# Optimization experiments

Measured on AMD Instinct MI355X. Metric: run time of the kernel, lower is better.

## Reference

```python
import jax, jax.numpy as jnp
import numpy as np

# Dims: B latent vectors processed through T sequential LALR-state calls.
B, T = 4096, 128      # batch of latent vecs, timesteps
NL = 256              # n_latent (scaled up from default 100)
NS = 64               # number of LALR states with learned layers
NO = 32               # output tokens per state (Linear(n_latent, n_out))
V = 64                # len(terminals): size of scattered output vector


def setup_inputs() -> dict:
    key = jax.random.key(0)
    ks = jax.random.split(key, 7)
    return {
        "latent0": jax.random.normal(ks[0], (B, NL), jnp.float32),
        "W1": jax.random.normal(ks[1], (NS, NL, NL), jnp.float32) / np.sqrt(NL).astype(np.float32),
        "b1": jax.random.normal(ks[2], (NS, NL), jnp.float32) * 0.01,
        "W2": jax.random.normal(ks[3], (NS, NO, NL), jnp.float32) / np.sqrt(NL).astype(np.float32),
        "b2": jax.random.normal(ks[4], (NS, NO), jnp.float32) * 0.01,
        "state_seq": jax.random.randint(ks[5], (T,), 0, NS, jnp.int32),
        "out_idx": jax.random.randint(ks[6], (NS, NO), 0, V, jnp.int32),
    }


def reference(latent0, W1, b1, W2, b2, state_seq, out_idx):
    """Per-timestep LALR state call:
       newlatent = tanh(Linear(x));
       probs     = softmax(Linear(newlatent));
       output    = IndicesExpansion: scatter probs into zeros(V) at out_idx[state].
    State weights are gathered by state id; batch is processed jointly."""
    def step(x, s):
        w1, bb1 = W1[s], b1[s]            # [NL,NL], [NL]
        w2, bb2 = W2[s], b2[s]            # [NO,NL], [NO]
        idx = out_idx[s]                  # [NO]
        x_new = jnp.tanh(x @ w1.T + bb1)                       # [B, NL]
        probs = jax.nn.softmax(x_new @ w2.T + bb2, axis=-1)    # [B, NO]
        # IndicesExpansionLayer: zero vector of size V, set vals at indices
        y = jnp.zeros((x.shape[0], V), x.dtype).at[:, idx].set(probs)
        return x_new, y

    final_latent, ys = jax.lax.scan(step, latent0, state_seq)  # ys: [T, B, V]
    return jnp.transpose(ys, (1, 0, 2))  # [B, T, V]
```

## Files before the change

kernel.cpp:

```cpp
#include <hip/hip_runtime.h>

#define B_  4096
#define T_  128
#define NL  256
#define NS  64
#define NO  32
#define V_  64
#define RB  16
#define NBLK (B_ / RB)

typedef __bf16 bf16;
typedef bf16  bf16x8 __attribute__((ext_vector_type(8)));
typedef bf16  bf16x4 __attribute__((ext_vector_type(4)));
typedef float f32x4  __attribute__((ext_vector_type(4)));

#define MF(a, b, c) __builtin_amdgcn_mfma_f32_16x16x32_bf16(a, b, c, 0, 0, 0)

#define LGKM_BARRIER() asm volatile("s_waitcnt lgkmcnt(0)\n\ts_barrier" ::: "memory")

#define GLOAD(dst, ptr, off) \
    asm volatile("global_load_dwordx4 %0, %1, off offset:" #off \
                 : "=v"(dst) : "v"(ptr))

template <int TSHIFT>
__global__ void split_w_frag(const float* __restrict__ src,
                             bf16* __restrict__ hi, bf16* __restrict__ lo,
                             int total4) {
    int t4 = blockIdx.x * blockDim.x + threadIdx.x;
    if (t4 >= total4) return;
    const int jb   = (t4 & 1) * 4;
    const int L    = (t4 >> 1) & 63;
    const int ks   = (t4 >> 7) & 7;
    const int rest = t4 >> 10;
    const int t    = rest & ((1 << TSHIFT) - 1);
    const int s    = rest >> TSHIFT;
    const int row  = ((s << TSHIFT) + t) * 16 + (L & 15);
    const int k    = ks * 32 + (L >> 4) * 8 + jb;
    const float4 v = *(const float4*)(src + (size_t)row * NL + k);
    float vv[4] = {v.x, v.y, v.z, v.w};
    bf16x4 h, l;
#pragma unroll
    for (int e = 0; e < 4; e++) {
        bf16 hh = (bf16)vv[e];
        h[e] = hh;
        l[e] = (bf16)(vv[e] - (float)hh);
    }
    *(bf16x4*)(hi + (size_t)t4 * 4) = h;
    *(bf16x4*)(lo + (size_t)t4 * 4) = l;
}

__global__ void inv_kernel(const int* __restrict__ out_idx, int* __restrict__ inv) {
    int t = blockIdx.x * blockDim.x + threadIdx.x;
    if (t >= NS * V_) return;
    int s = t >> 6, v = t & 63;
    int jf = -1;
#pragma unroll
    for (int j = 0; j < NO; j++)
        if (out_idx[(s << 5) | j] == v) jf = j;
    inv[t] = jf;
}

__device__ __forceinline__ float fast_tanh(float z) {
    float e = __expf(2.0f * z);
    return 1.0f - 2.0f / (e + 1.0f);
}

__device__ __forceinline__ int xaddr(int t, int q, int n) {
    return ((t >> 1) * 512) + (((t & 1) * 2 + (q >> 1)) * 128) + n * 8 + (q & 1) * 4;
}

__launch_bounds__(1024, 4)
__global__ void lalr_main(const float* __restrict__ latent0,
                          const float* __restrict__ b1,
                          const float* __restrict__ b2,
                          const int*   __restrict__ state_seq,
                          const int*   __restrict__ inv,
                          const bf16*  __restrict__ W1h, const bf16* __restrict__ W1l,
                          const bf16*  __restrict__ W2h, const bf16* __restrict__ W2l,
                          float* __restrict__ out) {
    __shared__ bf16  xh[2][4096];
    __shared__ bf16  xl[2][4096];
    __shared__ float Sp[2][8][16][36];
    __shared__ float b1s[NS * NL];
    __shared__ float b2s[NS * NO];
    __shared__ int   invs[NS * V_];
    __shared__ int   sseq[T_];

    const int tid  = threadIdx.x;
    const int wave = tid >> 6;
    const int lane = tid & 63;
    const int n    = lane & 15;
    const int q    = lane >> 4;
    const int r0   = blockIdx.x * RB;
    const int t2   = wave & 1;
    const int ks2  = wave >> 1;

    for (int k = tid; k < NS * NL / 4; k += 1024)
        ((float4*)b1s)[k] = ((const float4*)b1)[k];
    if (tid < NS * NO / 4) ((float4*)b2s)[tid] = ((const float4*)b2)[tid];
    if (tid < NS * V_ / 4) ((int4*)invs)[tid] = ((const int4*)inv)[tid];
    if (tid < T_) sseq[tid] = state_seq[tid];

    {
        float4 v = *(const float4*)(latent0 + (size_t)(r0 + n) * NL + wave * 16 + q * 4);
        float vv[4] = {v.x, v.y, v.z, v.w};
        bf16x4 hv, lv;
#pragma unroll
        for (int e = 0; e < 4; e++) {
            bf16 hh = (bf16)vv[e];
            hv[e] = hh;
            lv[e] = (bf16)(vv[e] - (float)hv[e]);
        }
        const int a = xaddr(wave, q, n);
        *(bf16x4*)(&xh[0][a]) = hv;
        *(bf16x4*)(&xl[0][a]) = lv;
    }

    int s0 = state_seq[0], s1 = -1, s2 = -1;

    bf16x8 pwh0, pwh1, pwh2, pwh3, pwh4, pwh5, pwh6, pwh7;
    bf16x8 pwl0, pwl1, pwl2, pwl3, pwl4, pwl5, pwl6, pwl7;
    bf16x8 w2h2, w2l2;

    const size_t wfrag = (size_t)wave * 8 * 512 + lane * 8;

    {
        const bf16* h0 = W1h + (size_t)s0 * 16 * 8 * 512 + wfrag;
        const bf16* l0 = W1l + (size_t)s0 * 16 * 8 * 512 + wfrag;
        const bf16* h4 = h0 + 4 * 512;
        const bf16* l4 = l0 + 4 * 512;
        GLOAD(pwh0, h0, 0);    GLOAD(pwl0, l0, 0);
        GLOAD(pwh1, h0, 1024); GLOAD(pwl1, l0, 1024);
        GLOAD(pwh2, h0, 2048); GLOAD(pwl2, l0, 2048);
        GLOAD(pwh3, h0, 3072); GLOAD(pwl3, l0, 3072);
        GLOAD(pwh4, h4, 0);    GLOAD(pwl4, l4, 0);
        GLOAD(pwh5, h4, 1024); GLOAD(pwl5, l4, 1024);
        GLOAD(pwh6, h4, 2048); GLOAD(pwl6, l4, 2048);
        GLOAD(pwh7, h4, 3072); GLOAD(pwl7, l4, 3072);
        const bf16* c2h = W2h + (size_t)((s0 * 2 + t2) * 8 + ks2) * 512 + lane * 8;
        const bf16* c2l = W2l + (size_t)((s0 * 2 + t2) * 8 + ks2) * 512 + lane * 8;
        GLOAD(w2h2, c2h, 0);   GLOAD(w2l2, c2l, 0);
    }

    LGKM_BARRIER();

#define G1S(ks, ph, pl, off) {                                              \
        bf16x8 xa = *(const bf16x8*)(&xh[cur][ks * 512 + lane * 8]);        \
        bf16x8 xb = *(const bf16x8*)(&xl[cur][ks * 512 + lane * 8]);        \
        asm volatile("s_waitcnt vmcnt(16)" ::: "memory");                   \
        __builtin_amdgcn_sched_barrier(0);                                  \
        acc1 = MF(pwh##ks, xa, acc1);                                       \
        acc1 = MF(pwl##ks, xa, acc1);                                       \
        acc1 = MF(pwh##ks, xb, acc1);                                       \
        GLOAD(pwh##ks, ph, off);                                            \
        GLOAD(pwl##ks, pl, off);                                            \
    }

    for (int i = 0; i <= T_ + 1; i++) {
        const int ib  = i & 1;
        const int cur = ib;

        const int ns0 = (i + 1 < T_) ? sseq[i + 1] : -1;
        const int ls  = (ns0 >= 0) ? ns0 : 0;
        const bf16* nh0 = W1h + (size_t)ls * 16 * 8 * 512 + wfrag;
        const bf16* nl0 = W1l + (size_t)ls * 16 * 8 * 512 + wfrag;
        const bf16* nh4 = nh0 + 4 * 512;
        const bf16* nl4 = nl0 + 4 * 512;

        f32x4 acc1;
        if (s0 >= 0) {
            acc1 = (f32x4){0.f, 0.f, 0.f, 0.f};
            G1S(0, nh0, nl0, 0)
            G1S(1, nh0, nl0, 1024)
            G1S(2, nh0, nl0, 2048)
            G1S(3, nh0, nl0, 3072)
            G1S(4, nh4, nl4, 0)
            G1S(5, nh4, nl4, 1024)
            G1S(6, nh4, nl4, 2048)
            G1S(7, nh4, nl4, 3072)
        }

        if (s1 >= 0) {
            bf16x8 xa = *(const bf16x8*)(&xh[cur][ks2 * 512 + lane * 8]);
            bf16x8 xb = *(const bf16x8*)(&xl[cur][ks2 * 512 + lane * 8]);
            if (s0 >= 0) {
                asm volatile("s_waitcnt vmcnt(16)" ::: "memory");
            } else {
                asm volatile("s_waitcnt vmcnt(0)" ::: "memory");
            }
            __builtin_amdgcn_sched_barrier(0);
            f32x4 a2 = (f32x4){0.f, 0.f, 0.f, 0.f};
            a2 = MF(w2h2, xa, a2);
            a2 = MF(w2l2, xa, a2);
            a2 = MF(w2h2, xb, a2);
            if (ks2 == 0) {
                float4 bb = *(const float4*)(&b2s[s1 * NO + t2 * 16 + q * 4]);
                a2[0] += bb.x; a2[1] += bb.y; a2[2] += bb.z; a2[3] += bb.w;
            }
            *(f32x4*)(&Sp[ib][ks2][n][t2 * 16 + q * 4]) = a2;
        }
        if (s0 >= 0) {
            const bf16* n2h = W2h + (size_t)((s0 * 2 + t2) * 8 + ks2) * 512 + lane * 8;
            const bf16* n2l = W2l + (size_t)((s0 * 2 + t2) * 8 + ks2) * 512 + lane * 8;
            GLOAD(w2h2, n2h, 0);
            GLOAD(w2l2, n2l, 0);
        }

        if (s2 >= 0 && tid < 256) {
            const int r  = tid >> 4;
            const int j0 = tid & 15;
            const int pb = (i - 1) & 1;
            float v0 = 0.f, v1 = 0.f;
#pragma unroll
            for (int w = 0; w < 8; w++) {
                v0 += Sp[pb][w][r][j0];
                v1 += Sp[pb][w][r][j0 + 16];
            }
            float m = fmaxf(v0, v1);
#pragma unroll
            for (int d = 1; d < 16; d <<= 1) m = fmaxf(m, __shfl_xor(m, d));
            float e0 = __expf(v0 - m), e1 = __expf(v1 - m);
            float su = e0 + e1;
#pragma unroll
            for (int d = 1; d < 16; d <<= 1) su += __shfl_xor(su, d);
            float is = 1.0f / su;
            float p0 = e0 * is, p1 = e1 * is;
            const int gb = lane & 48;
            int4 iv4 = *(const int4*)(&invs[s2 * V_ + j0 * 4]);
            int ivv[4] = {iv4.x, iv4.y, iv4.z, iv4.w};
            float o[4];
#pragma unroll
            for (int e = 0; e < 4; e++) {
                float ga = __shfl(p0, gb + (ivv[e] & 15));
                float gc = __shfl(p1, gb + (ivv[e] & 15));
                o[e] = (ivv[e] < 0) ? 0.f : ((ivv[e] < 16) ? ga : gc);
            }
            *(float4*)(out + ((size_t)(r0 + r) * T_ + (i - 2)) * V_ + j0 * 4) = *(float4*)o;
        }

        if (s0 >= 0) {
            float4 bb = *(const float4*)(&b1s[s0 * NL + wave * 16 + q * 4]);
            float bv[4] = {bb.x, bb.y, bb.z, bb.w};
            bf16x4 hv, lv;
#pragma unroll
            for (int e = 0; e < 4; e++) {
                float h = fast_tanh(acc1[e] + bv[e]);
                bf16 hh = (bf16)h;
                hv[e] = hh;
                lv[e] = (bf16)(h - (float)hh);
            }
            const int a = xaddr(wave, q, n);
            *(bf16x4*)(&xh[cur ^ 1][a]) = hv;
            *(bf16x4*)(&xl[cur ^ 1][a]) = lv;
        }

        s2 = s1; s1 = s0; s0 = ns0;
        LGKM_BARRIER();
    }
#undef G1S
}

extern "C" void kernel_launch(void* const* d_in, const int* in_sizes, int n_in,
                              void* d_out, int out_size, void* d_ws, size_t ws_size,
                              hipStream_t stream) {
    const float* latent0   = (const float*)d_in[0];
    const float* W1        = (const float*)d_in[1];
    const float* b1        = (const float*)d_in[2];
    const float* W2        = (const float*)d_in[3];
    const float* b2        = (const float*)d_in[4];
    const int*   state_seq = (const int*)d_in[5];
    const int*   out_idx   = (const int*)d_in[6];
    float* out = (float*)d_out;

    bf16* W1h = (bf16*)d_ws;
    bf16* W1l = W1h + (size_t)NS * NL * NL;
    bf16* W2h = W1l + (size_t)NS * NL * NL;
    bf16* W2l = W2h + (size_t)NS * NO * NL;
    int*  inv = (int*)(W2l + (size_t)NS * NO * NL);

    const int n4_w1 = NS * NL * NL / 4;
    const int n4_w2 = NS * NO * NL / 4;
    split_w_frag<4><<<n4_w1 / 256, 256, 0, stream>>>(W1, W1h, W1l, n4_w1);
    split_w_frag<1><<<n4_w2 / 256, 256, 0, stream>>>(W2, W2h, W2l, n4_w2);
    inv_kernel<<<(NS * V_ + 255) / 256, 256, 0, stream>>>(out_idx, inv);

    lalr_main<<<NBLK, 1024, 0, stream>>>(latent0, b1, b2, state_seq, inv,
                                         W1h, W1l, W2h, W2l, out);
}
```

Before: 550.9 us.

## Prefetch LDS x-fragments ahead of MFMAs and spread softmax epilogue across all waves

The layer-1 MFMA chain now issues its LDS reads of the split-bf16 latent fragments two k-steps ahead in rotating registers, so LDS latency overlaps the matrix ops. The layer-2 fragment read is folded into the last stage. The softmax/scatter epilogue, previously done by only the first 256 threads with two logits each, now runs on all 16 waves, one row per wave and one logit per lane, with 32-wide shuffles and scalar output stores. This spreads the serial tail work evenly but adds register pressure and more shuffle steps per lane.

```diff
diff --git a/kernel.cpp b/kernel.cpp
--- a/kernel.cpp
+++ b/kernel.cpp
@@ -109,7 +109,7 @@
         for (int e = 0; e < 4; e++) {
             bf16 hh = (bf16)vv[e];
             hv[e] = hh;
-            lv[e] = (bf16)(vv[e] - (float)hv[e]);
+            lv[e] = (bf16)(vv[e] - (float)hh);
         }
         const int a = xaddr(wave, q, n);
         *(bf16x4*)(&xh[0][a]) = hv;
@@ -144,16 +144,18 @@
 
     LGKM_BARRIER();
 
-#define G1S(ks, ph, pl, off) {                                              \
-        bf16x8 xa = *(const bf16x8*)(&xh[cur][ks * 512 + lane * 8]);        \
-        bf16x8 xb = *(const bf16x8*)(&xl[cur][ks * 512 + lane * 8]);        \
+#define XRD(dst, arr, ks) dst = *(const bf16x8*)(&arr[cur][(ks) * 512 + lane * 8])
+
+#define G1S(ks, A, B, PH, PL, off, ...)                                     \
+    {                                                                       \
+        __VA_ARGS__                                                         \
         asm volatile("s_waitcnt vmcnt(16)" ::: "memory");                   \
         __builtin_amdgcn_sched_barrier(0);                                  \
-        acc1 = MF(pwh##ks, xa, acc1);                                       \
-        acc1 = MF(pwl##ks, xa, acc1);                                       \
-        acc1 = MF(pwh##ks, xb, acc1);                                       \
-        GLOAD(pwh##ks, ph, off);                                            \
-        GLOAD(pwl##ks, pl, off);                                            \
+        acc1 = MF(pwh##ks, A, acc1);                                        \
+        acc1 = MF(pwl##ks, A, acc1);                                        \
+        acc1 = MF(pwh##ks, B, acc1);                                        \
+        GLOAD(pwh##ks, PH, off);                                            \
+        GLOAD(pwl##ks, PL, off);                                            \
     }
 
     for (int i = 0; i <= T_ + 1; i++) {
@@ -167,37 +169,41 @@
         const bf16* nh4 = nh0 + 4 * 512;
         const bf16* nl4 = nl0 + 4 * 512;
 
+        bf16x8 g2a, g2b;
+
         f32x4 acc1;
         if (s0 >= 0) {
             acc1 = (f32x4){0.f, 0.f, 0.f, 0.f};
-            G1S(0, nh0, nl0, 0)
-            G1S(1, nh0, nl0, 1024)
-            G1S(2, nh0, nl0, 2048)
-            G1S(3, nh0, nl0, 3072)
-            G1S(4, nh4, nl4, 0)
-            G1S(5, nh4, nl4, 1024)
-            G1S(6, nh4, nl4, 2048)
-            G1S(7, nh4, nl4, 3072)
+            bf16x8 a0, b0, a1, b1v, a2, b2v;
+            XRD(a0, xh, 0); XRD(b0, xl, 0);
+            XRD(a1, xh, 1); XRD(b1v, xl, 1);
+            G1S(0, a0, b0,  nh0, nl0, 0,    XRD(a2, xh, 2); XRD(b2v, xl, 2);)
+            G1S(1, a1, b1v, nh0, nl0, 1024, XRD(a0, xh, 3); XRD(b0, xl, 3);)
+            G1S(2, a2, b2v, nh0, nl0, 2048, XRD(a1, xh, 4); XRD(b1v, xl, 4);)
+            G1S(3, a0, b0,  nh0, nl0, 3072, XRD(a2, xh, 5); XRD(b2v, xl, 5);)
+            G1S(4, a1, b1v, nh4, nl4, 0,    XRD(a0, xh, 6); XRD(b0, xl, 6);)
+            G1S(5, a2, b2v, nh4, nl4, 1024, XRD(a1, xh, 7); XRD(b1v, xl, 7);)
+            G1S(6, a0, b0,  nh4, nl4, 2048, XRD(g2a, xh, ks2); XRD(g2b, xl, ks2);)
+            G1S(7, a1, b1v, nh4, nl4, 3072, )
         }
 
         if (s1 >= 0) {
-            bf16x8 xa = *(const bf16x8*)(&xh[cur][ks2 * 512 + lane * 8]);
-            bf16x8 xb = *(const bf16x8*)(&xl[cur][ks2 * 512 + lane * 8]);
+            if (s0 < 0) { XRD(g2a, xh, ks2); XRD(g2b, xl, ks2); }
             if (s0 >= 0) {
                 asm volatile("s_waitcnt vmcnt(16)" ::: "memory");
             } else {
                 asm volatile("s_waitcnt vmcnt(0)" ::: "memory");
             }
             __builtin_amdgcn_sched_barrier(0);
-            f32x4 a2 = (f32x4){0.f, 0.f, 0.f, 0.f};
-            a2 = MF(w2h2, xa, a2);
-            a2 = MF(w2l2, xa, a2);
-            a2 = MF(w2h2, xb, a2);
+            f32x4 a2acc = (f32x4){0.f, 0.f, 0.f, 0.f};
+            a2acc = MF(w2h2, g2a, a2acc);
+            a2acc = MF(w2l2, g2a, a2acc);
+            a2acc = MF(w2h2, g2b, a2acc);
             if (ks2 == 0) {
                 float4 bb = *(const float4*)(&b2s[s1 * NO + t2 * 16 + q * 4]);
-                a2[0] += bb.x; a2[1] += bb.y; a2[2] += bb.z; a2[3] += bb.w;
+                a2acc[0] += bb.x; a2acc[1] += bb.y; a2acc[2] += bb.z; a2acc[3] += bb.w;
             }
-            *(f32x4*)(&Sp[ib][ks2][n][t2 * 16 + q * 4]) = a2;
+            *(f32x4*)(&Sp[ib][ks2][n][t2 * 16 + q * 4]) = a2acc;
         }
         if (s0 >= 0) {
             const bf16* n2h = W2h + (size_t)((s0 * 2 + t2) * 8 + ks2) * 512 + lane * 8;
@@ -206,36 +212,23 @@
             GLOAD(w2l2, n2l, 0);
         }
 
-        if (s2 >= 0 && tid < 256) {
-            const int r  = tid >> 4;
-            const int j0 = tid & 15;
+        if (s2 >= 0) {
             const int pb = (i - 1) & 1;
-            float v0 = 0.f, v1 = 0.f;
-#pragma unroll
-            for (int w = 0; w < 8; w++) {
-                v0 += Sp[pb][w][r][j0];
-                v1 += Sp[pb][w][r][j0 + 16];
-            }
-            float m = fmaxf(v0, v1);
-#pragma unroll
-            for (int d = 1; d < 16; d <<= 1) m = fmaxf(m, __shfl_xor(m, d));
-            float e0 = __expf(v0 - m), e1 = __expf(v1 - m);
-            float su = e0 + e1;
-#pragma unroll
-            for (int d = 1; d < 16; d <<= 1) su += __shfl_xor(su, d);
-            float is = 1.0f / su;
-            float p0 = e0 * is, p1 = e1 * is;
-            const int gb = lane & 48;
-            int4 iv4 = *(const int4*)(&invs[s2 * V_ + j0 * 4]);
-            int ivv[4] = {iv4.x, iv4.y, iv4.z, iv4.w};
-            float o[4];
-#pragma unroll
-            for (int e = 0; e < 4; e++) {
-                float ga = __shfl(p0, gb + (ivv[e] & 15));
-                float gc = __shfl(p1, gb + (ivv[e] & 15));
-                o[e] = (ivv[e] < 0) ? 0.f : ((ivv[e] < 16) ? ga : gc);
-            }
-            *(float4*)(out + ((size_t)(r0 + r) * T_ + (i - 2)) * V_ + j0 * 4) = *(float4*)o;
+            const int c  = lane & 31;
+            float v = 0.f;
+#pragma unroll
+            for (int w8 = 0; w8 < 8; w8++) v += Sp[pb][w8][wave][c];
+            float m = v;
+#pragma unroll
+            for (int d = 1; d < 32; d <<= 1) m = fmaxf(m, __shfl_xor(m, d));
+            float e = __expf(v - m);
+            float su = e;
+#pragma unroll
+            for (int d = 1; d < 32; d <<= 1) su += __shfl_xor(su, d);
+            float p = e / su;
+            int iv = invs[s2 * V_ + lane];
+            float g = __shfl(p, iv & 31);
+            out[((size_t)(r0 + wave) * T_ + (i - 2)) * V_ + lane] = (iv < 0) ? 0.f : g;
         }
 
         if (s0 >= 0) {
@@ -258,6 +251,7 @@
         LGKM_BARRIER();
     }
 #undef G1S
+#undef XRD
 }
 
 extern "C" void kernel_launch(void* const* d_in, const int* in_sizes, int n_in,
```

Result: slower. 600.0 us (+8.9%).

## Process 32 rows per block, reusing each weight fragment across two row halves

Applied to the files above, without the earlier changes.

Doubles rows per block from 16 to 32 so every W1/W2 fragment loaded from global memory feeds two MFMA row tiles. This halves per-row weight traffic and halves the block count. W1 prefetch becomes a half-current/half-next split of 4 register slots with retuned vmcnt waits. The b1 bias is no longer staged in LDS but loaded per step from global, and the tanh write-back is moved before the softmax stage. It risks lower parallelism (128 blocks on many CUs), higher LDS use, and fragile hand-counted vmcnt values.

```diff
diff --git a/kernel.cpp b/kernel.cpp
--- a/kernel.cpp
+++ b/kernel.cpp
@@ -6,7 +6,7 @@
 #define NS  64
 #define NO  32
 #define V_  64
-#define RB  16
+#define RB  32
 #define NBLK (B_ / RB)
 
 typedef __bf16 bf16;
@@ -65,8 +65,8 @@
     return 1.0f - 2.0f / (e + 1.0f);
 }
 
-__device__ __forceinline__ int xaddr(int t, int q, int n) {
-    return ((t >> 1) * 512) + (((t & 1) * 2 + (q >> 1)) * 128) + n * 8 + (q & 1) * 4;
+__device__ __forceinline__ int xaddr32(int t, int q, int n, int rh) {
+    return (t >> 1) * 1024 + rh * 512 + ((t & 1) * 2 + (q >> 1)) * 128 + n * 8 + (q & 1) * 4;
 }
 
 __launch_bounds__(1024, 4)
@@ -78,10 +78,9 @@
                           const bf16*  __restrict__ W1h, const bf16* __restrict__ W1l,
                           const bf16*  __restrict__ W2h, const bf16* __restrict__ W2l,
                           float* __restrict__ out) {
-    __shared__ bf16  xh[2][4096];
-    __shared__ bf16  xl[2][4096];
-    __shared__ float Sp[2][8][16][36];
-    __shared__ float b1s[NS * NL];
+    __shared__ bf16  xh[2][8192];
+    __shared__ bf16  xl[2][8192];
+    __shared__ float Sp[2][4][32][36];
     __shared__ float b2s[NS * NO];
     __shared__ int   invs[NS * V_];
     __shared__ int   sseq[T_];
@@ -93,67 +92,71 @@
     const int q    = lane >> 4;
     const int r0   = blockIdx.x * RB;
     const int t2   = wave & 1;
-    const int ks2  = wave >> 1;
-
-    for (int k = tid; k < NS * NL / 4; k += 1024)
-        ((float4*)b1s)[k] = ((const float4*)b1)[k];
+    const int rh2  = (wave >> 1) & 1;
+    const int kp   = wave >> 2;
+    const int sa   = 2 * kp;
+
     if (tid < NS * NO / 4) ((float4*)b2s)[tid] = ((const float4*)b2)[tid];
     if (tid < NS * V_ / 4) ((int4*)invs)[tid] = ((const int4*)inv)[tid];
     if (tid < T_) sseq[tid] = state_seq[tid];
 
     {
-        float4 v = *(const float4*)(latent0 + (size_t)(r0 + n) * NL + wave * 16 + q * 4);
-        float vv[4] = {v.x, v.y, v.z, v.w};
-        bf16x4 hv, lv;
+        const float* pa = latent0 + (size_t)(r0 + n) * NL + wave * 16 + q * 4;
+        float4 va = *(const float4*)pa;
+        float4 vb = *(const float4*)(pa + 16 * NL);
+        float fa[4] = {va.x, va.y, va.z, va.w};
+        float fb[4] = {vb.x, vb.y, vb.z, vb.w};
+        bf16x4 hva, lva, hvb, lvb;
 #pragma unroll
         for (int e = 0; e < 4; e++) {
-            bf16 hh = (bf16)vv[e];
-            hv[e] = hh;
-            lv[e] = (bf16)(vv[e] - (float)hv[e]);
-        }
-        const int a = xaddr(wave, q, n);
-        *(bf16x4*)(&xh[0][a]) = hv;
-        *(bf16x4*)(&xl[0][a]) = lv;
+            bf16 ha = (bf16)fa[e]; hva[e] = ha; lva[e] = (bf16)(fa[e] - (float)ha);
+            bf16 hb = (bf16)fb[e]; hvb[e] = hb; lvb[e] = (bf16)(fb[e] - (float)hb);
+        }
+        const int a0 = xaddr32(wave, q, n, 0);
+        const int a1 = xaddr32(wave, q, n, 1);
+        *(bf16x4*)(&xh[0][a0]) = hva; *(bf16x4*)(&xl[0][a0]) = lva;
+        *(bf16x4*)(&xh[0][a1]) = hvb; *(bf16x4*)(&xl[0][a1]) = lvb;
     }
 
     int s0 = state_seq[0], s1 = -1, s2 = -1;
 
-    bf16x8 pwh0, pwh1, pwh2, pwh3, pwh4, pwh5, pwh6, pwh7;
-    bf16x8 pwl0, pwl1, pwl2, pwl3, pwl4, pwl5, pwl6, pwl7;
-    bf16x8 w2h2, w2l2;
+    bf16x8 pwh0, pwh1, pwh2, pwh3;
+    bf16x8 pwl0, pwl1, pwl2, pwl3;
+    bf16x8 w2ha, w2la, w2hb, w2lb;
+    f32x4  b1v;
 
     const size_t wfrag = (size_t)wave * 8 * 512 + lane * 8;
 
     {
-        const bf16* h0 = W1h + (size_t)s0 * 16 * 8 * 512 + wfrag;
-        const bf16* l0 = W1l + (size_t)s0 * 16 * 8 * 512 + wfrag;
-        const bf16* h4 = h0 + 4 * 512;
-        const bf16* l4 = l0 + 4 * 512;
-        GLOAD(pwh0, h0, 0);    GLOAD(pwl0, l0, 0);
-        GLOAD(pwh1, h0, 1024); GLOAD(pwl1, l0, 1024);
-        GLOAD(pwh2, h0, 2048); GLOAD(pwl2, l0, 2048);
-        GLOAD(pwh3, h0, 3072); GLOAD(pwl3, l0, 3072);
-        GLOAD(pwh4, h4, 0);    GLOAD(pwl4, l4, 0);
-        GLOAD(pwh5, h4, 1024); GLOAD(pwl5, l4, 1024);
-        GLOAD(pwh6, h4, 2048); GLOAD(pwl6, l4, 2048);
-        GLOAD(pwh7, h4, 3072); GLOAD(pwl7, l4, 3072);
-        const bf16* c2h = W2h + (size_t)((s0 * 2 + t2) * 8 + ks2) * 512 + lane * 8;
-        const bf16* c2l = W2l + (size_t)((s0 * 2 + t2) * 8 + ks2) * 512 + lane * 8;
-        GLOAD(w2h2, c2h, 0);   GLOAD(w2l2, c2l, 0);
+        const bf16* cbh = W1h + (size_t)s0 * 16 * 8 * 512 + wfrag + 4 * 512;
+        const bf16* cbl = W1l + (size_t)s0 * 16 * 8 * 512 + wfrag + 4 * 512;
+        GLOAD(pwh0, cbh, -4096); GLOAD(pwl0, cbl, -4096);
+        GLOAD(pwh1, cbh, -3072); GLOAD(pwl1, cbl, -3072);
+        GLOAD(pwh2, cbh, -2048); GLOAD(pwl2, cbl, -2048);
+        GLOAD(pwh3, cbh, -1024); GLOAD(pwl3, cbl, -1024);
+        const bf16* c2h = W2h + (size_t)((s0 * 2 + t2) * 8 + sa) * 512 + lane * 8;
+        const bf16* c2l = W2l + (size_t)((s0 * 2 + t2) * 8 + sa) * 512 + lane * 8;
+        GLOAD(w2ha, c2h, 0);    GLOAD(w2la, c2l, 0);
+        GLOAD(w2hb, c2h, 1024); GLOAD(w2lb, c2l, 1024);
     }
 
     LGKM_BARRIER();
 
-#define G1S(ks, ph, pl, off) {                                              \
-        bf16x8 xa = *(const bf16x8*)(&xh[cur][ks * 512 + lane * 8]);        \
-        bf16x8 xb = *(const bf16x8*)(&xl[cur][ks * 512 + lane * 8]);        \
-        asm volatile("s_waitcnt vmcnt(16)" ::: "memory");                   \
+#define G1S(c, s, BH, BL, OFF, CNT) {                                       \
+        bf16x8 xa0 = *(const bf16x8*)(xbh + (c) * 1024);                    \
+        bf16x8 xb0 = *(const bf16x8*)(xbl + (c) * 1024);                    \
+        bf16x8 xa1 = *(const bf16x8*)(xbh + (c) * 1024 + 512);              \
+        bf16x8 xb1 = *(const bf16x8*)(xbl + (c) * 1024 + 512);              \
+        asm volatile("s_waitcnt vmcnt(" #CNT ")" ::: "memory");             \
         __builtin_amdgcn_sched_barrier(0);                                  \
-        acc1 = MF(pwh##ks, xa, acc1);                                       \
-        acc1 = MF(pwl##ks, xa, acc1);                                       \
-        acc1 = MF(pwh##ks, xb, acc1);                                       \
-        GLOAD(pwh##ks, ph, off);                                            \
-        GLOAD(pwl##ks, pl, off);                                            \
+        acc1a = MF(pwh##s, xa0, acc1a);                                     \
+        acc1b = MF(pwh##s, xa1, acc1b);                                     \
+        acc1a = MF(pwl##s, xa0, acc1a);                                     \
+        acc1b = MF(pwl##s, xa1, acc1b);                                     \
+        acc1a = MF(pwh##s, xb0, acc1a);                                     \
+        acc1b = MF(pwh##s, xb1, acc1b);                                     \
+        GLOAD(pwh##s, BH, OFF);                                             \
+        GLOAD(pwl##s, BL, OFF);                                             \
     }
 
     for (int i = 0; i <= T_ + 1; i++) {
@@ -162,59 +165,95 @@
 
         const int ns0 = (i + 1 < T_) ? sseq[i + 1] : -1;
         const int ls  = (ns0 >= 0) ? ns0 : 0;
-        const bf16* nh0 = W1h + (size_t)ls * 16 * 8 * 512 + wfrag;
-        const bf16* nl0 = W1l + (size_t)ls * 16 * 8 * 512 + wfrag;
-        const bf16* nh4 = nh0 + 4 * 512;
-        const bf16* nl4 = nl0 + 4 * 512;
-
-        f32x4 acc1;
+        const bf16* cbh = W1h + (size_t)s0 * 16 * 8 * 512 + wfrag + 2048;
+        const bf16* cbl = W1l + (size_t)s0 * 16 * 8 * 512 + wfrag + 2048;
+        const bf16* nbh = W1h + (size_t)ls * 16 * 8 * 512 + wfrag + 2048;
+        const bf16* nbl = W1l + (size_t)ls * 16 * 8 * 512 + wfrag + 2048;
+        const bf16* xbh = &xh[cur][lane * 8];
+        const bf16* xbl = &xl[cur][lane * 8];
+
         if (s0 >= 0) {
-            acc1 = (f32x4){0.f, 0.f, 0.f, 0.f};
-            G1S(0, nh0, nl0, 0)
-            G1S(1, nh0, nl0, 1024)
-            G1S(2, nh0, nl0, 2048)
-            G1S(3, nh0, nl0, 3072)
-            G1S(4, nh4, nl4, 0)
-            G1S(5, nh4, nl4, 1024)
-            G1S(6, nh4, nl4, 2048)
-            G1S(7, nh4, nl4, 3072)
+            const float* pb1 = b1 + (size_t)s0 * NL + wave * 16 + q * 4;
+            GLOAD(b1v, pb1, 0);
+        }
+
+        f32x4 acc1a, acc1b;
+        if (s0 >= 0) {
+            acc1a = (f32x4){0.f, 0.f, 0.f, 0.f};
+            acc1b = (f32x4){0.f, 0.f, 0.f, 0.f};
+            G1S(0, 0, cbh, cbl, 0,     11)
+            G1S(1, 1, cbh, cbl, 1024,  11)
+            G1S(2, 2, cbh, cbl, 2048,  11)
+            G1S(3, 3, cbh, cbl, 3072,  11)
+            G1S(4, 0, nbh, nbl, -4096, 5)
+            G1S(5, 1, nbh, nbl, -3072, 5)
+            G1S(6, 2, nbh, nbl, -2048, 5)
+            G1S(7, 3, nbh, nbl, -1024, 5)
         }
 
         if (s1 >= 0) {
-            bf16x8 xa = *(const bf16x8*)(&xh[cur][ks2 * 512 + lane * 8]);
-            bf16x8 xb = *(const bf16x8*)(&xl[cur][ks2 * 512 + lane * 8]);
+            const bf16* g2h = xbh + sa * 1024 + rh2 * 512;
+            const bf16* g2l = xbl + sa * 1024 + rh2 * 512;
+            bf16x8 xa0 = *(const bf16x8*)(g2h);
+            bf16x8 xb0 = *(const bf16x8*)(g2l);
+            bf16x8 xa1 = *(const bf16x8*)(g2h + 1024);
+            bf16x8 xb1 = *(const bf16x8*)(g2l + 1024);
             if (s0 >= 0) {
-                asm volatile("s_waitcnt vmcnt(16)" ::: "memory");
+                asm volatile("s_waitcnt vmcnt(17)" ::: "memory");
             } else {
                 asm volatile("s_waitcnt vmcnt(0)" ::: "memory");
             }
             __builtin_amdgcn_sched_barrier(0);
             f32x4 a2 = (f32x4){0.f, 0.f, 0.f, 0.f};
-            a2 = MF(w2h2, xa, a2);
-            a2 = MF(w2l2, xa, a2);
-            a2 = MF(w2h2, xb, a2);
-            if (ks2 == 0) {
+            a2 = MF(w2ha, xa0, a2);
+            a2 = MF(w2la, xa0, a2);
+            a2 = MF(w2ha, xb0, a2);
+            a2 = MF(w2hb, xa1, a2);
+            a2 = MF(w2lb, xa1, a2);
+            a2 = MF(w2hb, xb1, a2);
+            if (kp == 0) {
                 float4 bb = *(const float4*)(&b2s[s1 * NO + t2 * 16 + q * 4]);
                 a2[0] += bb.x; a2[1] += bb.y; a2[2] += bb.z; a2[3] += bb.w;
             }
-            *(f32x4*)(&Sp[ib][ks2][n][t2 * 16 + q * 4]) = a2;
+            *(f32x4*)(&Sp[ib][kp][rh2 * 16 + n][t2 * 16 + q * 4]) = a2;
         }
         if (s0 >= 0) {
-            const bf16* n2h = W2h + (size_t)((s0 * 2 + t2) * 8 + ks2) * 512 + lane * 8;
-            const bf16* n2l = W2l + (size_t)((s0 * 2 + t2) * 8 + ks2) * 512 + lane * 8;
-            GLOAD(w2h2, n2h, 0);
-            GLOAD(w2l2, n2l, 0);
-        }
-
-        if (s2 >= 0 && tid < 256) {
+            const bf16* n2h = W2h + (size_t)((s0 * 2 + t2) * 8 + sa) * 512 + lane * 8;
+            const bf16* n2l = W2l + (size_t)((s0 * 2 + t2) * 8 + sa) * 512 + lane * 8;
+            GLOAD(w2ha, n2h, 0);
+            GLOAD(w2la, n2l, 0);
+            GLOAD(w2hb, n2h, 1024);
+            GLOAD(w2lb, n2l, 1024);
+        }
+
+        if (s0 >= 0) {
+            asm volatile("s_waitcnt vmcnt(20)" ::: "memory");
+            __builtin_amdgcn_sched_barrier(0);
+            bf16x4 hva, lva, hvb, lvb;
+#pragma unroll
+            for (int e = 0; e < 4; e++) {
+                float ha = fast_tanh(acc1a[e] + b1v[e]);
+                bf16 hh = (bf16)ha;
+                hva[e] = hh; lva[e] = (bf16)(ha - (float)hh);
+                float hb = fast_tanh(acc1b[e] + b1v[e]);
+                bf16 hh2 = (bf16)hb;
+                hvb[e] = hh2; lvb[e] = (bf16)(hb - (float)hh2);
+            }
+            const int a0 = xaddr32(wave, q, n, 0);
+            const int a1 = xaddr32(wave, q, n, 1);
+            *(bf16x4*)(&xh[cur ^ 1][a0]) = hva; *(bf16x4*)(&xl[cur ^ 1][a0]) = lva;
+            *(bf16x4*)(&xh[cur ^ 1][a1]) = hvb; *(bf16x4*)(&xl[cur ^ 1][a1]) = lvb;
+        }
+
+        if (s2 >= 0 && tid < 512) {
             const int r  = tid >> 4;
             const int j0 = tid & 15;
             const int pb = (i - 1) & 1;
             float v0 = 0.f, v1 = 0.f;
 #pragma unroll
-            for (int w = 0; w < 8; w++) {
-                v0 += Sp[pb][w][r][j0];
-                v1 += Sp[pb][w][r][j0 + 16];
+            for (int kq = 0; kq < 4; kq++) {
+                v0 += Sp[pb][kq][r][j0];
+                v1 += Sp[pb][kq][r][j0 + 16];
             }
             float m = fmaxf(v0, v1);
 #pragma unroll
@@ -236,22 +275,6 @@
                 o[e] = (ivv[e] < 0) ? 0.f : ((ivv[e] < 16) ? ga : gc);
             }
             *(float4*)(out + ((size_t)(r0 + r) * T_ + (i - 2)) * V_ + j0 * 4) = *(float4*)o;
-        }
-
-        if (s0 >= 0) {
-            float4 bb = *(const float4*)(&b1s[s0 * NL + wave * 16 + q * 4]);
-            float bv[4] = {bb.x, bb.y, bb.z, bb.w};
-            bf16x4 hv, lv;
-#pragma unroll
-            for (int e = 0; e < 4; e++) {
-                float h = fast_tanh(acc1[e] + bv[e]);
-                bf16 hh = (bf16)h;
-                hv[e] = hh;
-                lv[e] = (bf16)(h - (float)hh);
-            }
-            const int a = xaddr(wave, q, n);
-            *(bf16x4*)(&xh[cur ^ 1][a]) = hv;
-            *(bf16x4*)(&xl[cur ^ 1][a]) = lv;
         }
 
         s2 = s1; s1 = s0; s0 = ns0;
```

Measured after the change: 574.9 us. +4.3%, slower.
